# Kernel tuning notes

Hardware: AMD Instinct MI355X
Metric: run time of the kernel (lower is better)

The kernel has to match this reference:

```python
import jax, jax.numpy as jnp
import numpy as np

# dims: T time steps, B batch, F clinical features, H GRU hidden, NH heads, DFF ffn dim, AH single-attn hidden
T, B, F, H, NH, DFF, AH = 128, 256, 76, 64, 4, 256, 8


def setup_inputs() -> dict:
    key = jax.random.key(0)
    ks = jax.random.split(key, 32)
    s = 0.1
    def u(k, shape):
        return jax.random.uniform(k, shape, jnp.float32, -s, s)
    return {
        "x": jax.random.normal(ks[0], (T, B, F), jnp.float32),
        # per-feature GRU(1, H) weight stacks (torch gate order: r, z, n)
        "gru_w_ih": u(ks[1], (F, 3 * H)),          # input dim is 1 -> squeezed
        "gru_w_hh": u(ks[2], (F, 3 * H, H)),
        "gru_b_ih": jnp.zeros((F, 3 * H), jnp.float32),
        "gru_b_hh": jnp.zeros((F, 3 * H), jnp.float32),
        # per-feature SingleAttention('new', time_aware) params
        "att_Wt": u(ks[3], (F, H, AH)),
        "att_Wx": u(ks[4], (F, H, AH)),
        "att_rate": jnp.full((F,), 0.8, jnp.float32),
        # multi-head self-attention over the feature axis
        "mha_wq": u(ks[5], (H, H)), "mha_bq": jnp.zeros((H,), jnp.float32),
        "mha_wk": u(ks[6], (H, H)), "mha_bk": jnp.zeros((H,), jnp.float32),
        "mha_wv": u(ks[7], (H, H)), "mha_bv": jnp.zeros((H,), jnp.float32),
        "mha_wo": u(ks[8], (H, H)), "mha_bo": jnp.zeros((H,), jnp.float32),
        # position-wise feed forward
        "ffn_w1": u(ks[9], (H, DFF)), "ffn_b1": jnp.zeros((DFF,), jnp.float32),
        "ffn_w2": u(ks[10], (DFF, H)), "ffn_b2": jnp.zeros((H,), jnp.float32),
        # FinalAttentionQKV ('mul')
        "fa_wq": u(ks[11], (H, H)), "fa_bq": jnp.zeros((H,), jnp.float32),
        "fa_wk": u(ks[12], (H, H)), "fa_bk": jnp.zeros((H,), jnp.float32),
        "fa_wv": u(ks[13], (H, H)), "fa_bv": jnp.zeros((H,), jnp.float32),
        # output head
        "out0_w": u(ks[14], (H, H)), "out0_b": jnp.zeros((H,), jnp.float32),
        "out1_w": u(ks[15], (H, 1)), "out1_b": jnp.zeros((1,), jnp.float32),
    }


def reference(x, gru_w_ih, gru_w_hh, gru_b_ih, gru_b_hh,
              att_Wt, att_Wx, att_rate,
              mha_wq, mha_bq, mha_wk, mha_bk, mha_wv, mha_bv, mha_wo, mha_bo,
              ffn_w1, ffn_b1, ffn_w2, ffn_b2,
              fa_wq, fa_bq, fa_wk, fa_bk, fa_wv, fa_bv,
              out0_w, out0_b, out1_w, out1_b):
    # x: (T, B, F); torch permutes to (B, T, F)
    Ts, Bsz, Fd = x.shape
    Hd = gru_w_hh.shape[-1]
    dk = Hd // NH

    # ---- all F GRU(1,H) channels fused into one scan (vectorized over F) ----
    xs = jnp.transpose(x, (0, 2, 1))  # (T, F, B)

    def step(h, x_t):  # h: (F,B,H), x_t: (F,B)
        gx = x_t[:, :, None] * gru_w_ih[:, None, :] + gru_b_ih[:, None, :]      # (F,B,3H)
        gh = jnp.einsum('fbh,fgh->fbg', h, gru_w_hh) + gru_b_hh[:, None, :]     # (F,B,3H)
        rx, zx, nx = jnp.split(gx, 3, axis=-1)
        rh, zh, nh = jnp.split(gh, 3, axis=-1)
        r = jax.nn.sigmoid(rx + rh)
        z = jax.nn.sigmoid(zx + zh)
        n = jnp.tanh(nx + r * nh)
        h_new = (1.0 - z) * n + z * h
        return h_new, h_new

    h0 = jnp.zeros((Fd, Bsz, Hd), x.dtype)
    _, hs = jax.lax.scan(step, h0, xs)        # (T, F, B, H)
    hs = jnp.transpose(hs, (1, 2, 0, 3))       # (F, B, T, H)

    # ---- per-feature SingleAttention, type='new', time-aware ----
    q = jnp.einsum('fbh,fha->fba', hs[:, :, -1, :], att_Wt)   # (F,B,AH)
    k = jnp.einsum('fbth,fha->fbta', hs, att_Wx)              # (F,B,T,AH)
    dp = jnp.einsum('fba,fbta->fbt', q, k)                    # (F,B,T)
    sig = jax.nn.sigmoid(dp)
    decay = jnp.arange(Ts, 0, -1, dtype=x.dtype)              # T..1 (time_decays + 1)
    denom = jax.nn.sigmoid(att_rate)[:, None, None] * (jnp.log(2.72 + (1.0 - sig)) * decay)
    e = jax.nn.relu(sig / denom)
    a = jax.nn.softmax(e, axis=-1)
    emb = jnp.einsum('fbt,fbth->bfh', a, hs)                  # (B, F, H)

    def lin(t, w, b):
        return t @ w + b

    # ---- multi-head self-attention over the F axis + residual ----
    # NOTE: original lambda ignores its (layernormed) argument, so LN is dead code.
    def heads(t):
        return t.reshape(Bsz, Fd, NH, dk).transpose(0, 2, 1, 3)
    qh = heads(lin(emb, mha_wq, mha_bq))
    kh = heads(lin(emb, mha_wk, mha_bk))
    vh = heads(lin(emb, mha_wv, mha_bv))
    scores = jnp.einsum('bhqd,bhkd->bhqk', qh, kh) / jnp.sqrt(jnp.asarray(dk, x.dtype))
    attn = jax.nn.softmax(scores, axis=-1)
    ctx = jnp.einsum('bhqk,bhkd->bhqd', attn, vh).transpose(0, 2, 1, 3).reshape(Bsz, Fd, Hd)
    ctx = emb + lin(ctx, mha_wo, mha_bo)

    # ---- position-wise feed-forward + residual ----
    ctx = ctx + lin(jax.nn.relu(lin(ctx, ffn_w1, ffn_b1)), ffn_w2, ffn_b2)

    # ---- FinalAttentionQKV, type='mul' ----
    fq = lin(ctx[:, -1, :], fa_wq, fa_bq)      # (B,H)
    fk = lin(ctx, fa_wk, fa_bk)                # (B,F,H)
    fv = lin(ctx, fa_wv, fa_bv)                # (B,F,H)
    fe = jnp.einsum('bfh,bh->bf', fk, fq)
    fa_w = jax.nn.softmax(fe, axis=1)
    v = jnp.einsum('bf,bfh->bh', fa_w, fv)     # (B,H)

    # ---- output head ----
    out = jax.nn.sigmoid(lin(jax.nn.relu(lin(v, out0_w, out0_b)), out1_w, out1_b))
    return out  # (B, 1)
```

## Files before the change

### kernel.cpp

```cpp
#include <hip/hip_runtime.h>
#include <hip/hip_bf16.h>
#include <cstdint>
#include <cstddef>

#define TT 128
#define BBATCH 256
#define FFEAT 76
#define HDIM 64
#define NHEAD 4
#define DKH 16
#define DFF1 256
#define AH1 8
#define NROWS (BBATCH * FFEAT)

#define LOG2E 1.4426950408889634f

typedef __attribute__((ext_vector_type(8))) short bf16x8;
typedef __attribute__((ext_vector_type(4))) float f32x4;

__device__ __forceinline__ float fast_sigmoid(float v) {
    float p = __builtin_amdgcn_exp2f(-v * LOG2E);
    return __builtin_amdgcn_rcpf(1.0f + p);
}
__device__ __forceinline__ float fast_tanh(float v) {
    float p = __builtin_amdgcn_exp2f(v * (2.0f * LOG2E));
    return 1.0f - 2.0f * __builtin_amdgcn_rcpf(1.0f + p);
}
__device__ __forceinline__ short f2bf(float x) {
    __hip_bfloat16 h = __float2bfloat16(x);
    return *reinterpret_cast<short*>(&h);
}

__global__ __launch_bounds__(512, 2) void gru_mfma_kernel(
    const float* __restrict__ x, const float* __restrict__ w_ih,
    const float* __restrict__ w_hh, const float* __restrict__ b_ih,
    const float* __restrict__ b_hh, int f_base, __hip_bfloat16* __restrict__ hs)
{
    const int f_loc = blockIdx.y;
    const int f     = f_base + f_loc;
    const int b0    = blockIdx.x * 64;
    const int tid   = threadIdx.x;
    const int wave  = tid >> 6;
    const int lane  = tid & 63;
    const int col   = lane & 15;
    const int quad  = lane >> 4;
    const int ug    = wave & 3;
    const int mt0   = (wave >> 2) * 2;
    const int u     = ug * 16 + col;

    __shared__ __align__(16) short h_lds[2][64][72];
    __shared__ __align__(16) float x_lds[TT][64];

    for (int i = tid; i < TT * 64; i += 512) {
        int t = i >> 6, b = i & 63;
        x_lds[t][b] = x[(size_t)t * BBATCH * FFEAT + (size_t)(b0 + b) * FFEAT + f];
    }
    for (int i = tid; i < 64 * 72; i += 512) ((short*)h_lds[0])[i] = 0;

    bf16x8 bfr[3][2];
    {
        const float* whh_f = w_hh + (size_t)f * 192 * 64;
        #pragma unroll
        for (int gi = 0; gi < 3; ++gi) {
            const float* row = whh_f + (size_t)(gi * 64 + u) * 64;
            #pragma unroll
            for (int kq = 0; kq < 2; ++kq) {
                const float* src = row + kq * 32 + quad * 8;
                bf16x8 fr;
                #pragma unroll
                for (int j = 0; j < 8; ++j) fr[j] = f2bf(src[j]);
                bfr[gi][kq] = fr;
            }
        }
    }
    const float wihr  = w_ih[f*192 + u];
    const float wihz  = w_ih[f*192 + 64 + u];
    const float wihn  = w_ih[f*192 + 128 + u];
    const float brz_r = b_ih[f*192 + u]      + b_hh[f*192 + u];
    const float brz_z = b_ih[f*192 + 64 + u] + b_hh[f*192 + 64 + u];
    const float bih_n = b_ih[f*192 + 128 + u];
    const float bhh_n = b_hh[f*192 + 128 + u];

    float hprev[2][4] = {{0.f,0.f,0.f,0.f},{0.f,0.f,0.f,0.f}};
    __syncthreads();

    int p = 0;
    for (int t = 0; t < TT; ++t) {
        bf16x8 afr[2][2];
        #pragma unroll
        for (int mi = 0; mi < 2; ++mi)
            #pragma unroll
            for (int kq = 0; kq < 2; ++kq)
                afr[mi][kq] = *(const bf16x8*)&h_lds[p][(mt0+mi)*16 + col][kq*32 + quad*8];

        f32x4 acc[2][3];
        #pragma unroll
        for (int mi = 0; mi < 2; ++mi)
            #pragma unroll
            for (int gi = 0; gi < 3; ++gi) {
                f32x4 a = {0.f, 0.f, 0.f, 0.f};
                a = __builtin_amdgcn_mfma_f32_16x16x32_bf16(afr[mi][0], bfr[gi][0], a, 0, 0, 0);
                a = __builtin_amdgcn_mfma_f32_16x16x32_bf16(afr[mi][1], bfr[gi][1], a, 0, 0, 0);
                acc[mi][gi] = a;
            }

        #pragma unroll
        for (int mi = 0; mi < 2; ++mi) {
            const int brow = (mt0 + mi) * 16 + quad * 4;
            float4 xv = *(const float4*)&x_lds[t][brow];
            #pragma unroll
            for (int r = 0; r < 4; ++r) {
                float xb = (&xv.x)[r];
                float R  = acc[mi][0][r] + fmaf(xb, wihr, brz_r);
                float Z  = acc[mi][1][r] + fmaf(xb, wihz, brz_z);
                float NH = acc[mi][2][r] + bhh_n;
                float NX = fmaf(xb, wihn, bih_n);
                float rg = fast_sigmoid(R);
                float zg = fast_sigmoid(Z);
                float ng = fast_tanh(fmaf(rg, NH, NX));
                float hn = fmaf(zg, hprev[mi][r] - ng, ng);
                hprev[mi][r] = hn;
                short hb = f2bf(hn);
                h_lds[p^1][brow + r][u] = hb;
                hs[(((size_t)f_loc * BBATCH + b0 + brow + r) * TT + t) * HDIM + u] =
                    *reinterpret_cast<__hip_bfloat16*>(&hb);
            }
        }
        __syncthreads();
        p ^= 1;
    }
}

__global__ __launch_bounds__(128) void attn_kernel(
    const __hip_bfloat16* __restrict__ hs, const float* __restrict__ Wt,
    const float* __restrict__ Wx, const float* __restrict__ rate,
    int f_base, float* __restrict__ emb)
{
    const int b     = blockIdx.x;
    const int f_loc = blockIdx.y;
    const int f     = f_base + f_loc;
    const int tid   = threadIdx.x;

    __shared__ float h_s[TT][HDIM + 1];
    __shared__ float wx_s[HDIM][AH1];
    __shared__ float wt_s[HDIM][AH1];
    __shared__ float q_s[AH1];
    __shared__ float a_s[TT];
    __shared__ float redm[2], redp[2];
    __shared__ float partial_s[HDIM];

    for (int i = tid; i < HDIM * AH1; i += 128) {
        ((float*)wx_s)[i] = Wx[(size_t)f * HDIM * AH1 + i];
        ((float*)wt_s)[i] = Wt[(size_t)f * HDIM * AH1 + i];
    }

    float hreg[HDIM];
    {
        const __hip_bfloat16* src = hs + (((size_t)f_loc * BBATCH + b) * TT + tid) * HDIM;
        #pragma unroll
        for (int c = 0; c < 8; ++c) {
            uint4 u4 = ((const uint4*)src)[c];
            unsigned vals[4] = {u4.x, u4.y, u4.z, u4.w};
            #pragma unroll
            for (int pp = 0; pp < 4; ++pp) {
                hreg[c*8 + 2*pp]     = __uint_as_float(vals[pp] << 16);
                hreg[c*8 + 2*pp + 1] = __uint_as_float(vals[pp] & 0xffff0000u);
            }
        }
        #pragma unroll
        for (int j = 0; j < HDIM; ++j) h_s[tid][j] = hreg[j];
    }
    __syncthreads();

    if (tid < AH1) {
        float acc = 0.f;
        #pragma unroll
        for (int j = 0; j < HDIM; ++j) acc += h_s[TT-1][j] * wt_s[j][tid];
        q_s[tid] = acc;
    }
    __syncthreads();

    float k[AH1];
    #pragma unroll
    for (int a = 0; a < AH1; ++a) k[a] = 0.f;
    #pragma unroll
    for (int j = 0; j < HDIM; ++j) {
        float hv = hreg[j];
        #pragma unroll
        for (int a = 0; a < AH1; ++a) k[a] = fmaf(hv, wx_s[j][a], k[a]);
    }
    float dp = 0.f;
    #pragma unroll
    for (int a = 0; a < AH1; ++a) dp += k[a] * q_s[a];

    float sig   = fast_sigmoid(dp);
    float rs    = fast_sigmoid(rate[f]);
    float decay = (float)(TT - tid);
    float denom = rs * (__logf(2.72f + (1.0f - sig)) * decay);
    float e = fmaxf(sig / denom, 0.0f);

    float m = e;
    #pragma unroll
    for (int off = 32; off > 0; off >>= 1) m = fmaxf(m, __shfl_xor(m, off, 64));
    if ((tid & 63) == 0) redm[tid >> 6] = m;
    __syncthreads();
    m = fmaxf(redm[0], redm[1]);
    float pr = __builtin_amdgcn_exp2f((e - m) * LOG2E);
    float s = pr;
    #pragma unroll
    for (int off = 32; off > 0; off >>= 1) s += __shfl_xor(s, off, 64);
    if ((tid & 63) == 0) redp[tid >> 6] = s;
    __syncthreads();
    s = redp[0] + redp[1];
    a_s[tid] = pr / s;
    __syncthreads();

    const int j    = tid & 63;
    const int half = tid >> 6;
    float acc = 0.f;
    const int t0 = half * 64;
    #pragma unroll 8
    for (int t2 = t0; t2 < t0 + 64; ++t2)
        acc = fmaf(a_s[t2], h_s[t2][j], acc);
    if (half) partial_s[j] = acc;
    __syncthreads();
    if (!half) emb[((size_t)b * FFEAT + f) * HDIM + j] = acc + partial_s[j];
}

struct GemmP {
    const float* X;
    const float* W[3];
    const float* B[3];
    const float* R;
    float* Y[3];
    int K;
    int Nfull;
    int act;
};

__global__ __launch_bounds__(256) void gemm_kernel(GemmP A)
{
    __shared__ float xs[64][65];
    __shared__ float ws[64][68];

    const int tid = threadIdx.x;
    const int tx  = tid & 15;
    const int ty  = tid >> 4;
    const int m0  = blockIdx.x * 64;
    const int n0  = blockIdx.y * 64;
    const int z   = blockIdx.z;

    const float* W = A.W[z];
    const float* Bv = A.B[z];
    float* Y = A.Y[z];
    const int K = A.K, Nfull = A.Nfull;

    float acc[4][4];
    #pragma unroll
    for (int i = 0; i < 4; ++i)
        #pragma unroll
        for (int j = 0; j < 4; ++j) acc[i][j] = 0.f;

    for (int kc = 0; kc < K; kc += 64) {
        for (int s = tid; s < 1024; s += 256) {
            int row = s >> 4, c4 = s & 15;
            float4 xv = *(const float4*)&A.X[(size_t)(m0 + row) * K + kc + 4*c4];
            xs[row][4*c4+0] = xv.x; xs[row][4*c4+1] = xv.y;
            xs[row][4*c4+2] = xv.z; xs[row][4*c4+3] = xv.w;
            float4 wv = *(const float4*)&W[(size_t)(kc + row) * Nfull + n0 + 4*c4];
            *(float4*)&ws[row][4*c4] = wv;
        }
        __syncthreads();
        #pragma unroll 16
        for (int k = 0; k < 64; ++k) {
            float a0 = xs[4*ty+0][k], a1 = xs[4*ty+1][k];
            float a2 = xs[4*ty+2][k], a3 = xs[4*ty+3][k];
            float4 wv = *(const float4*)&ws[k][4*tx];
            #pragma unroll
            for (int j = 0; j < 4; ++j) {
                float wj = (&wv.x)[j];
                acc[0][j] = fmaf(a0, wj, acc[0][j]);
                acc[1][j] = fmaf(a1, wj, acc[1][j]);
                acc[2][j] = fmaf(a2, wj, acc[2][j]);
                acc[3][j] = fmaf(a3, wj, acc[3][j]);
            }
        }
        __syncthreads();
    }

    float4 bias = *(const float4*)&Bv[n0 + 4*tx];
    #pragma unroll
    for (int i = 0; i < 4; ++i) {
        int row = m0 + 4*ty + i;
        float4 v;
        v.x = acc[i][0] + bias.x; v.y = acc[i][1] + bias.y;
        v.z = acc[i][2] + bias.z; v.w = acc[i][3] + bias.w;
        if (A.act) {
            v.x = fmaxf(v.x, 0.f); v.y = fmaxf(v.y, 0.f);
            v.z = fmaxf(v.z, 0.f); v.w = fmaxf(v.w, 0.f);
        }
        if (A.R) {
            float4 r4 = *(const float4*)&A.R[(size_t)row * Nfull + n0 + 4*tx];
            v.x += r4.x; v.y += r4.y; v.z += r4.z; v.w += r4.w;
        }
        *(float4*)&Y[(size_t)row * Nfull + n0 + 4*tx] = v;
    }
}

__global__ __launch_bounds__(256) void mha_core_kernel(
    const float* __restrict__ q, const float* __restrict__ k,
    const float* __restrict__ v, float* __restrict__ ctx)
{
    const int b  = blockIdx.x;
    const int hh = blockIdx.y;
    const int tid = threadIdx.x;

    __shared__ float qs[FFEAT][17];
    __shared__ float ks[FFEAT][17];
    __shared__ float vs[FFEAT][17];
    __shared__ float ps[FFEAT][77];

    for (int idx = tid; idx < FFEAT * DKH; idx += 256) {
        int i = idx >> 4, c = idx & 15;
        size_t g = ((size_t)b * FFEAT + i) * HDIM + hh * DKH + c;
        qs[i][c] = q[g]; ks[i][c] = k[g]; vs[i][c] = v[g];
    }
    __syncthreads();

    for (int idx = tid; idx < FFEAT * FFEAT; idx += 256) {
        int i = idx / FFEAT, j = idx % FFEAT;
        float acc = 0.f;
        #pragma unroll
        for (int c = 0; c < DKH; ++c) acc = fmaf(qs[i][c], ks[j][c], acc);
        ps[i][j] = acc * 0.25f;
    }
    __syncthreads();

    if (tid < FFEAT) {
        float mm = ps[tid][0];
        #pragma unroll 4
        for (int j = 1; j < FFEAT; ++j) mm = fmaxf(mm, ps[tid][j]);
        float ss = 0.f;
        #pragma unroll 4
        for (int j = 0; j < FFEAT; ++j) {
            float pv = __builtin_amdgcn_exp2f((ps[tid][j] - mm) * LOG2E);
            ps[tid][j] = pv; ss += pv;
        }
        float inv = 1.0f / ss;
        #pragma unroll 4
        for (int j = 0; j < FFEAT; ++j) ps[tid][j] *= inv;
    }
    __syncthreads();

    for (int idx = tid; idx < FFEAT * DKH; idx += 256) {
        int i = idx >> 4, c = idx & 15;
        float acc = 0.f;
        #pragma unroll 4
        for (int j = 0; j < FFEAT; ++j) acc = fmaf(ps[i][j], vs[j][c], acc);
        ctx[((size_t)b * FFEAT + i) * HDIM + hh * DKH + c] = acc;
    }
}

__global__ __launch_bounds__(128) void final_kernel(
    const float* __restrict__ ctx3, const float* __restrict__ fk,
    const float* __restrict__ fv,
    const float* __restrict__ faq, const float* __restrict__ fabq,
    const float* __restrict__ o0w, const float* __restrict__ o0b,
    const float* __restrict__ o1w, const float* __restrict__ o1b,
    float* __restrict__ out)
{
    const int b = blockIdx.x;
    const int tid = threadIdx.x;

    __shared__ float last[HDIM];
    __shared__ float fqs[HDIM];
    __shared__ float sm[FFEAT];
    __shared__ float vv[HDIM];
    __shared__ float hh[HDIM];
    __shared__ float redm[2], redp[2];

    if (tid < HDIM) last[tid] = ctx3[((size_t)b * FFEAT + FFEAT - 1) * HDIM + tid];
    __syncthreads();
    if (tid < HDIM) {
        float acc = fabq[tid];
        #pragma unroll 8
        for (int j = 0; j < HDIM; ++j) acc = fmaf(last[j], faq[j * HDIM + tid], acc);
        fqs[tid] = acc;
    }
    __syncthreads();

    float e = -3.0e38f;
    if (tid < FFEAT) {
        const float4* kr = (const float4*)&fk[((size_t)b * FFEAT + tid) * HDIM];
        float acc = 0.f;
        #pragma unroll
        for (int c4 = 0; c4 < 16; ++c4) {
            float4 kv = kr[c4];
            acc = fmaf(kv.x, fqs[4*c4+0], acc);
            acc = fmaf(kv.y, fqs[4*c4+1], acc);
            acc = fmaf(kv.z, fqs[4*c4+2], acc);
            acc = fmaf(kv.w, fqs[4*c4+3], acc);
        }
        e = acc;
    }
    float m = e;
    #pragma unroll
    for (int off = 32; off > 0; off >>= 1) m = fmaxf(m, __shfl_xor(m, off, 64));
    if ((tid & 63) == 0) redm[tid >> 6] = m;
    __syncthreads();
    m = fmaxf(redm[0], redm[1]);
    float p = (tid < FFEAT) ? __builtin_amdgcn_exp2f((e - m) * LOG2E) : 0.f;
    float s = p;
    #pragma unroll
    for (int off = 32; off > 0; off >>= 1) s += __shfl_xor(s, off, 64);
    if ((tid & 63) == 0) redp[tid >> 6] = s;
    __syncthreads();
    s = redp[0] + redp[1];
    if (tid < FFEAT) sm[tid] = p / s;
    __syncthreads();

    if (tid < HDIM) {
        float acc = 0.f;
        for (int ff = 0; ff < FFEAT; ++ff)
            acc = fmaf(sm[ff], fv[((size_t)b * FFEAT + ff) * HDIM + tid], acc);
        vv[tid] = acc;
    }
    __syncthreads();
    if (tid < HDIM) {
        float acc = o0b[tid];
        #pragma unroll 8
        for (int j = 0; j < HDIM; ++j) acc = fmaf(vv[j], o0w[j * HDIM + tid], acc);
        hh[tid] = fmaxf(acc, 0.f);
    }
    __syncthreads();
    if (tid < 64) {
        float t = hh[tid] * o1w[tid];
        #pragma unroll
        for (int off = 32; off > 0; off >>= 1) t += __shfl_xor(t, off, 64);
        if (tid == 0) out[b] = fast_sigmoid(t + o1b[0]);
    }
}

__global__ void ws_report_kernel(float* out, int n, float ws_mib) {
    int i = blockIdx.x * blockDim.x + threadIdx.x;
    if (i < n) out[i] = ws_mib;
}

extern "C" void kernel_launch(void* const* d_in, const int* in_sizes, int n_in,
                              void* d_out, int out_size, void* d_ws, size_t ws_size,
                              hipStream_t stream)
{
    const float* x     = (const float*)d_in[0];
    const float* w_ih  = (const float*)d_in[1];
    const float* w_hh  = (const float*)d_in[2];
    const float* b_ih  = (const float*)d_in[3];
    const float* b_hh  = (const float*)d_in[4];
    const float* attWt = (const float*)d_in[5];
    const float* attWx = (const float*)d_in[6];
    const float* attRt = (const float*)d_in[7];
    const float* wq    = (const float*)d_in[8];
    const float* bq    = (const float*)d_in[9];
    const float* wk    = (const float*)d_in[10];
    const float* bk    = (const float*)d_in[11];
    const float* wv    = (const float*)d_in[12];
    const float* bv    = (const float*)d_in[13];
    const float* wo    = (const float*)d_in[14];
    const float* bo    = (const float*)d_in[15];
    const float* w1    = (const float*)d_in[16];
    const float* b1    = (const float*)d_in[17];
    const float* w2    = (const float*)d_in[18];
    const float* b2    = (const float*)d_in[19];
    const float* faq   = (const float*)d_in[20];
    const float* fabq  = (const float*)d_in[21];
    const float* fak   = (const float*)d_in[22];
    const float* fabk  = (const float*)d_in[23];
    const float* fav   = (const float*)d_in[24];
    const float* fabv  = (const float*)d_in[25];
    const float* o0w   = (const float*)d_in[26];
    const float* o0b   = (const float*)d_in[27];
    const float* o1w   = (const float*)d_in[28];
    const float* o1b   = (const float*)d_in[29];
    float* out = (float*)d_out;

    const size_t emb_bytes  = (size_t)NROWS * HDIM * 4;
    const size_t R64        = (size_t)NROWS * HDIM;
    const size_t tail_bytes = 12 * R64 * 4;

    const int chunk_opts[6] = {76, 38, 19, 4, 2, 1};
    int FC = 0;
    for (int i = 0; i < 6; ++i) {
        size_t hs_b = (size_t)chunk_opts[i] * BBATCH * TT * HDIM * 2;
        size_t scratch = hs_b > tail_bytes ? hs_b : tail_bytes;
        if (emb_bytes + scratch <= ws_size) { FC = chunk_opts[i]; break; }
    }
    if (FC == 0) {
        ws_report_kernel<<<dim3((out_size + 255) / 256), dim3(256), 0, stream>>>(
            out, out_size, (float)((double)ws_size / (1024.0 * 1024.0)));
        return;
    }

    float* emb = (float*)d_ws;
    char*  scratch = (char*)d_ws + emb_bytes;
    __hip_bfloat16* hs = (__hip_bfloat16*)scratch;

    for (int f0 = 0; f0 < FFEAT; f0 += FC) {
        int fc = (FFEAT - f0 < FC) ? (FFEAT - f0) : FC;
        gru_mfma_kernel<<<dim3(4, fc), dim3(512), 0, stream>>>(
            x, w_ih, w_hh, b_ih, b_hh, f0, hs);
        attn_kernel<<<dim3(BBATCH, fc), dim3(128), 0, stream>>>(
            hs, attWt, attWx, attRt, f0, emb);
    }

    float* ts   = (float*)scratch;
    float* q    = ts;
    float* k    = ts + 1*R64;
    float* v    = ts + 2*R64;
    float* ctx  = ts + 3*R64;
    float* ctx2 = ts + 4*R64;
    float* hid  = ts + 5*R64;
    float* ctx3 = ts + 9*R64;
    float* fk   = ts + 10*R64;
    float* fv   = ts + 11*R64;

    const int MB = NROWS / 64;

    {
        GemmP A = { emb, {wq, wk, wv}, {bq, bk, bv}, nullptr, {q, k, v}, 64, 64, 0 };
        gemm_kernel<<<dim3(MB, 1, 3), dim3(256), 0, stream>>>(A);
    }
    mha_core_kernel<<<dim3(BBATCH, NHEAD), dim3(256), 0, stream>>>(q, k, v, ctx);
    {
        GemmP A = { ctx, {wo, nullptr, nullptr}, {bo, nullptr, nullptr}, emb,
                    {ctx2, nullptr, nullptr}, 64, 64, 0 };
        gemm_kernel<<<dim3(MB, 1, 1), dim3(256), 0, stream>>>(A);
    }
    {
        GemmP A = { ctx2, {w1, nullptr, nullptr}, {b1, nullptr, nullptr}, nullptr,
                    {hid, nullptr, nullptr}, 64, 256, 1 };
        gemm_kernel<<<dim3(MB, 4, 1), dim3(256), 0, stream>>>(A);
    }
    {
        GemmP A = { hid, {w2, nullptr, nullptr}, {b2, nullptr, nullptr}, ctx2,
                    {ctx3, nullptr, nullptr}, 256, 64, 0 };
        gemm_kernel<<<dim3(MB, 1, 1), dim3(256), 0, stream>>>(A);
    }
    {
        GemmP A = { ctx3, {fak, fav, nullptr}, {fabk, fabv, nullptr}, nullptr,
                    {fk, fv, nullptr}, 64, 64, 0 };
        gemm_kernel<<<dim3(MB, 1, 2), dim3(256), 0, stream>>>(A);
    }
    final_kernel<<<dim3(BBATCH), dim3(128), 0, stream>>>(
        ctx3, fk, fv, faq, fabq, o0w, o0b, o1w, o1b, out);
}
```

Before: 694.1 us.

## Make GRU waves independent and fold attention query into per-batch weight vector

The GRU kernel now gives each wave 16 batch rows and all 192 gate columns, so each wave keeps its own hidden state in LDS and the per-step block-wide barrier goes away. hs is stored time-major, written as 16-byte vectors one step late, and biases are preloaded into the MFMA accumulators. At the end the GRU kernel computes the last-step query and folds it with Wx into a per-(batch, feature) 64-vector, so the attention kernel only needs one dot product per time step instead of the full key projection. Attention runs as a single 64-thread wave with shuffle-only reductions. The cost is higher register pressure (24 B fragments per lane), fewer threads per GRU block, and strided per-timestep reads in the attention kernel.

```diff
diff --git a/kernel.cpp b/kernel.cpp
--- a/kernel.cpp
+++ b/kernel.cpp
@@ -30,201 +30,223 @@
     __hip_bfloat16 h = __float2bfloat16(x);
     return *reinterpret_cast<short*>(&h);
 }
-
-__global__ __launch_bounds__(512, 2) void gru_mfma_kernel(
+__device__ __forceinline__ float bf2f(unsigned short s) {
+    return __uint_as_float(((unsigned)s) << 16);
+}
+
+__global__ __launch_bounds__(256) void gru_scan_kernel(
     const float* __restrict__ x, const float* __restrict__ w_ih,
     const float* __restrict__ w_hh, const float* __restrict__ b_ih,
-    const float* __restrict__ b_hh, int f_base, __hip_bfloat16* __restrict__ hs)
+    const float* __restrict__ b_hh, const float* __restrict__ Wt,
+    const float* __restrict__ Wx, int f_base,
+    __hip_bfloat16* __restrict__ hs, float* __restrict__ wtil)
 {
     const int f_loc = blockIdx.y;
     const int f     = f_base + f_loc;
-    const int b0    = blockIdx.x * 64;
+    const int bblk  = blockIdx.x * 64;
     const int tid   = threadIdx.x;
     const int wave  = tid >> 6;
     const int lane  = tid & 63;
-    const int col   = lane & 15;
-    const int quad  = lane >> 4;
-    const int ug    = wave & 3;
-    const int mt0   = (wave >> 2) * 2;
-    const int u     = ug * 16 + col;
-
-    __shared__ __align__(16) short h_lds[2][64][72];
-    __shared__ __align__(16) float x_lds[TT][64];
-
-    for (int i = tid; i < TT * 64; i += 512) {
+    const int c     = lane & 15;
+    const int q     = lane >> 4;
+    const int b0    = bblk + wave * 16;
+
+    __shared__ float x_lds[TT][64];
+    __shared__ float wt_s[64][8];
+    __shared__ float wx_s[64][8];
+    __shared__ short hx[4][16][72];
+    __shared__ float q_s[4][16][8];
+
+    for (int i = tid; i < TT * 64; i += 256) {
         int t = i >> 6, b = i & 63;
-        x_lds[t][b] = x[(size_t)t * BBATCH * FFEAT + (size_t)(b0 + b) * FFEAT + f];
-    }
-    for (int i = tid; i < 64 * 72; i += 512) ((short*)h_lds[0])[i] = 0;
-
-    bf16x8 bfr[3][2];
+        x_lds[t][b] = x[((size_t)t * BBATCH + bblk + b) * FFEAT + f];
+    }
+    for (int i = tid; i < 512; i += 256) {
+        ((float*)wt_s)[i] = Wt[(size_t)f * 512 + i];
+        ((float*)wx_s)[i] = Wx[(size_t)f * 512 + i];
+    }
+    for (int i = lane; i < 16 * 72; i += 64) ((short*)hx[wave])[i] = 0;
+    __syncthreads();
+
+    bf16x8 bfr[12][2];
     {
         const float* whh_f = w_hh + (size_t)f * 192 * 64;
         #pragma unroll
-        for (int gi = 0; gi < 3; ++gi) {
-            const float* row = whh_f + (size_t)(gi * 64 + u) * 64;
+        for (int nt = 0; nt < 12; ++nt) {
+            const float* row = whh_f + (size_t)(nt * 16 + c) * 64;
             #pragma unroll
             for (int kq = 0; kq < 2; ++kq) {
-                const float* src = row + kq * 32 + quad * 8;
                 bf16x8 fr;
                 #pragma unroll
-                for (int j = 0; j < 8; ++j) fr[j] = f2bf(src[j]);
-                bfr[gi][kq] = fr;
+                for (int j = 0; j < 8; ++j) fr[j] = f2bf(row[kq * 32 + q * 8 + j]);
+                bfr[nt][kq] = fr;
             }
         }
     }
-    const float wihr  = w_ih[f*192 + u];
-    const float wihz  = w_ih[f*192 + 64 + u];
-    const float wihn  = w_ih[f*192 + 128 + u];
-    const float brz_r = b_ih[f*192 + u]      + b_hh[f*192 + u];
-    const float brz_z = b_ih[f*192 + 64 + u] + b_hh[f*192 + 64 + u];
-    const float bih_n = b_ih[f*192 + 128 + u];
-    const float bhh_n = b_hh[f*192 + 128 + u];
-
-    float hprev[2][4] = {{0.f,0.f,0.f,0.f},{0.f,0.f,0.f,0.f}};
-    __syncthreads();
-
-    int p = 0;
+    float wihr[4], wihz[4], wihn[4], bR[4], bZ[4], bNX[4], bNH[4];
+    #pragma unroll
+    for (int g = 0; g < 4; ++g) {
+        int u = g * 16 + c;
+        wihr[g] = w_ih[f*192 + u];
+        wihz[g] = w_ih[f*192 + 64 + u];
+        wihn[g] = w_ih[f*192 + 128 + u];
+        bR[g]  = b_ih[f*192 + u]      + b_hh[f*192 + u];
+        bZ[g]  = b_ih[f*192 + 64 + u] + b_hh[f*192 + 64 + u];
+        bNX[g] = b_ih[f*192 + 128 + u];
+        bNH[g] = b_hh[f*192 + 128 + u];
+    }
+
+    float hprev[4][4];
+    #pragma unroll
+    for (int g = 0; g < 4; ++g)
+        #pragma unroll
+        for (int r = 0; r < 4; ++r) hprev[g][r] = 0.f;
+
+    short* hs_s = (short*)hs + (size_t)f_loc * TT * BBATCH * HDIM;
+
     for (int t = 0; t < TT; ++t) {
-        bf16x8 afr[2][2];
-        #pragma unroll
-        for (int mi = 0; mi < 2; ++mi)
-            #pragma unroll
-            for (int kq = 0; kq < 2; ++kq)
-                afr[mi][kq] = *(const bf16x8*)&h_lds[p][(mt0+mi)*16 + col][kq*32 + quad*8];
-
-        f32x4 acc[2][3];
-        #pragma unroll
-        for (int mi = 0; mi < 2; ++mi)
-            #pragma unroll
-            for (int gi = 0; gi < 3; ++gi) {
-                f32x4 a = {0.f, 0.f, 0.f, 0.f};
-                a = __builtin_amdgcn_mfma_f32_16x16x32_bf16(afr[mi][0], bfr[gi][0], a, 0, 0, 0);
-                a = __builtin_amdgcn_mfma_f32_16x16x32_bf16(afr[mi][1], bfr[gi][1], a, 0, 0, 0);
-                acc[mi][gi] = a;
-            }
-
-        #pragma unroll
-        for (int mi = 0; mi < 2; ++mi) {
-            const int brow = (mt0 + mi) * 16 + quad * 4;
-            float4 xv = *(const float4*)&x_lds[t][brow];
+        bf16x8 a0 = *(const bf16x8*)&hx[wave][c][q * 8];
+        bf16x8 a1 = *(const bf16x8*)&hx[wave][c][32 + q * 8];
+        if (t > 0) {
+            short* dst = hs_s + ((size_t)(t - 1) * BBATCH + b0 + c) * HDIM + q * 8;
+            *(bf16x8*)dst = a0;
+            *(bf16x8*)(dst + 32) = a1;
+        }
+
+        f32x4 acc[12];
+        #pragma unroll
+        for (int g = 0; g < 4; ++g) {
+            acc[g]     = f32x4{bR[g],  bR[g],  bR[g],  bR[g]};
+            acc[g + 4] = f32x4{bZ[g],  bZ[g],  bZ[g],  bZ[g]};
+            acc[g + 8] = f32x4{bNH[g], bNH[g], bNH[g], bNH[g]};
+        }
+        #pragma unroll
+        for (int nt = 0; nt < 12; ++nt) {
+            acc[nt] = __builtin_amdgcn_mfma_f32_16x16x32_bf16(a0, bfr[nt][0], acc[nt], 0, 0, 0);
+            acc[nt] = __builtin_amdgcn_mfma_f32_16x16x32_bf16(a1, bfr[nt][1], acc[nt], 0, 0, 0);
+        }
+
+        float4 xv = *(const float4*)&x_lds[t][wave * 16 + q * 4];
+        #pragma unroll
+        for (int g = 0; g < 4; ++g) {
             #pragma unroll
             for (int r = 0; r < 4; ++r) {
                 float xb = (&xv.x)[r];
-                float R  = acc[mi][0][r] + fmaf(xb, wihr, brz_r);
-                float Z  = acc[mi][1][r] + fmaf(xb, wihz, brz_z);
-                float NH = acc[mi][2][r] + bhh_n;
-                float NX = fmaf(xb, wihn, bih_n);
+                float R  = fmaf(xb, wihr[g], acc[g][r]);
+                float Z  = fmaf(xb, wihz[g], acc[g + 4][r]);
+                float NX = fmaf(xb, wihn[g], bNX[g]);
                 float rg = fast_sigmoid(R);
                 float zg = fast_sigmoid(Z);
-                float ng = fast_tanh(fmaf(rg, NH, NX));
-                float hn = fmaf(zg, hprev[mi][r] - ng, ng);
-                hprev[mi][r] = hn;
-                short hb = f2bf(hn);
-                h_lds[p^1][brow + r][u] = hb;
-                hs[(((size_t)f_loc * BBATCH + b0 + brow + r) * TT + t) * HDIM + u] =
-                    *reinterpret_cast<__hip_bfloat16*>(&hb);
+                float ng = fast_tanh(fmaf(rg, acc[g + 8][r], NX));
+                float hn = fmaf(zg, hprev[g][r] - ng, ng);
+                hprev[g][r] = hn;
+                hx[wave][q * 4 + r][g * 16 + c] = f2bf(hn);
             }
         }
-        __syncthreads();
-        p ^= 1;
-    }
-}
-
-__global__ __launch_bounds__(128) void attn_kernel(
-    const __hip_bfloat16* __restrict__ hs, const float* __restrict__ Wt,
-    const float* __restrict__ Wx, const float* __restrict__ rate,
-    int f_base, float* __restrict__ emb)
+    }
+    {
+        bf16x8 a0 = *(const bf16x8*)&hx[wave][c][q * 8];
+        bf16x8 a1 = *(const bf16x8*)&hx[wave][c][32 + q * 8];
+        short* dst = hs_s + ((size_t)(TT - 1) * BBATCH + b0 + c) * HDIM + q * 8;
+        *(bf16x8*)dst = a0;
+        *(bf16x8*)(dst + 32) = a1;
+    }
+
+    #pragma unroll
+    for (int rr = 0; rr < 2; ++rr) {
+        int role = rr * 64 + lane;
+        int b = role >> 3, a = role & 7;
+        float s = 0.f;
+        #pragma unroll 8
+        for (int j = 0; j < 64; ++j)
+            s = fmaf(bf2f((unsigned short)hx[wave][b][j]), wt_s[j][a], s);
+        q_s[wave][b][a] = s;
+    }
+    {
+        int b = lane >> 2, jb = (lane & 3) * 16;
+        float qreg[8];
+        #pragma unroll
+        for (int a = 0; a < 8; ++a) qreg[a] = q_s[wave][b][a];
+        float* wt_out = wtil + ((size_t)(b0 + b) * FFEAT + f) * HDIM + jb;
+        #pragma unroll
+        for (int j4 = 0; j4 < 4; ++j4) {
+            float4 v;
+            #pragma unroll
+            for (int jj = 0; jj < 4; ++jj) {
+                int j = jb + j4 * 4 + jj;
+                float s = 0.f;
+                #pragma unroll
+                for (int a = 0; a < 8; ++a) s = fmaf(wx_s[j][a], qreg[a], s);
+                (&v.x)[jj] = s;
+            }
+            *(float4*)&wt_out[j4 * 4] = v;
+        }
+    }
+}
+
+__global__ __launch_bounds__(64) void attn2_kernel(
+    const __hip_bfloat16* __restrict__ hs, const float* __restrict__ wtil,
+    const float* __restrict__ rate, int f_base, float* __restrict__ emb)
 {
     const int b     = blockIdx.x;
     const int f_loc = blockIdx.y;
     const int f     = f_base + f_loc;
-    const int tid   = threadIdx.x;
-
-    __shared__ float h_s[TT][HDIM + 1];
-    __shared__ float wx_s[HDIM][AH1];
-    __shared__ float wt_s[HDIM][AH1];
-    __shared__ float q_s[AH1];
+    const int lane  = threadIdx.x;
+
     __shared__ float a_s[TT];
-    __shared__ float redm[2], redp[2];
-    __shared__ float partial_s[HDIM];
-
-    for (int i = tid; i < HDIM * AH1; i += 128) {
-        ((float*)wx_s)[i] = Wx[(size_t)f * HDIM * AH1 + i];
-        ((float*)wt_s)[i] = Wt[(size_t)f * HDIM * AH1 + i];
-    }
-
-    float hreg[HDIM];
-    {
-        const __hip_bfloat16* src = hs + (((size_t)f_loc * BBATCH + b) * TT + tid) * HDIM;
-        #pragma unroll
-        for (int c = 0; c < 8; ++c) {
-            uint4 u4 = ((const uint4*)src)[c];
-            unsigned vals[4] = {u4.x, u4.y, u4.z, u4.w};
+
+    float wreg[64];
+    {
+        const float4* src = (const float4*)(wtil + ((size_t)b * FFEAT + f) * HDIM);
+        #pragma unroll
+        for (int i = 0; i < 16; ++i) {
+            float4 v = src[i];
+            wreg[4*i+0] = v.x; wreg[4*i+1] = v.y; wreg[4*i+2] = v.z; wreg[4*i+3] = v.w;
+        }
+    }
+    const float rs = fast_sigmoid(rate[f]);
+    const short* hsp = (const short*)hs + (size_t)f_loc * TT * BBATCH * HDIM;
+
+    float e[2];
+    #pragma unroll
+    for (int half = 0; half < 2; ++half) {
+        int t = half * 64 + lane;
+        const uint4* row = (const uint4*)(hsp + ((size_t)t * BBATCH + b) * HDIM);
+        float dp = 0.f;
+        #pragma unroll
+        for (int c4 = 0; c4 < 8; ++c4) {
+            uint4 u = row[c4];
+            unsigned vals[4] = {u.x, u.y, u.z, u.w};
             #pragma unroll
-            for (int pp = 0; pp < 4; ++pp) {
-                hreg[c*8 + 2*pp]     = __uint_as_float(vals[pp] << 16);
-                hreg[c*8 + 2*pp + 1] = __uint_as_float(vals[pp] & 0xffff0000u);
+            for (int p = 0; p < 4; ++p) {
+                dp = fmaf(__uint_as_float(vals[p] << 16),        wreg[c4*8 + 2*p],     dp);
+                dp = fmaf(__uint_as_float(vals[p] & 0xffff0000u), wreg[c4*8 + 2*p + 1], dp);
             }
         }
-        #pragma unroll
-        for (int j = 0; j < HDIM; ++j) h_s[tid][j] = hreg[j];
-    }
-    __syncthreads();
-
-    if (tid < AH1) {
-        float acc = 0.f;
-        #pragma unroll
-        for (int j = 0; j < HDIM; ++j) acc += h_s[TT-1][j] * wt_s[j][tid];
-        q_s[tid] = acc;
-    }
-    __syncthreads();
-
-    float k[AH1];
-    #pragma unroll
-    for (int a = 0; a < AH1; ++a) k[a] = 0.f;
-    #pragma unroll
-    for (int j = 0; j < HDIM; ++j) {
-        float hv = hreg[j];
-        #pragma unroll
-        for (int a = 0; a < AH1; ++a) k[a] = fmaf(hv, wx_s[j][a], k[a]);
-    }
-    float dp = 0.f;
-    #pragma unroll
-    for (int a = 0; a < AH1; ++a) dp += k[a] * q_s[a];
-
-    float sig   = fast_sigmoid(dp);
-    float rs    = fast_sigmoid(rate[f]);
-    float decay = (float)(TT - tid);
-    float denom = rs * (__logf(2.72f + (1.0f - sig)) * decay);
-    float e = fmaxf(sig / denom, 0.0f);
-
-    float m = e;
+        float sig = fast_sigmoid(dp);
+        float den = rs * (__logf(2.72f + (1.0f - sig)) * (float)(TT - t));
+        e[half] = fmaxf(sig / den, 0.0f);
+    }
+    float m = fmaxf(e[0], e[1]);
     #pragma unroll
     for (int off = 32; off > 0; off >>= 1) m = fmaxf(m, __shfl_xor(m, off, 64));
-    if ((tid & 63) == 0) redm[tid >> 6] = m;
-    __syncthreads();
-    m = fmaxf(redm[0], redm[1]);
-    float pr = __builtin_amdgcn_exp2f((e - m) * LOG2E);
-    float s = pr;
+    float p0 = __builtin_amdgcn_exp2f((e[0] - m) * LOG2E);
+    float p1 = __builtin_amdgcn_exp2f((e[1] - m) * LOG2E);
+    float s = p0 + p1;
     #pragma unroll
     for (int off = 32; off > 0; off >>= 1) s += __shfl_xor(s, off, 64);
-    if ((tid & 63) == 0) redp[tid >> 6] = s;
-    __syncthreads();
-    s = redp[0] + redp[1];
-    a_s[tid] = pr / s;
-    __syncthreads();
-
-    const int j    = tid & 63;
-    const int half = tid >> 6;
+    float inv = __builtin_amdgcn_rcpf(s);
+    a_s[lane]      = p0 * inv;
+    a_s[lane + 64] = p1 * inv;
+
+    const int j = lane;
     float acc = 0.f;
-    const int t0 = half * 64;
     #pragma unroll 8
-    for (int t2 = t0; t2 < t0 + 64; ++t2)
-        acc = fmaf(a_s[t2], h_s[t2][j], acc);
-    if (half) partial_s[j] = acc;
-    __syncthreads();
-    if (!half) emb[((size_t)b * FFEAT + f) * HDIM + j] = acc + partial_s[j];
+    for (int t = 0; t < TT; ++t) {
+        unsigned short hv = *(const unsigned short*)(hsp + ((size_t)t * BBATCH + b) * HDIM + j);
+        acc = fmaf(a_s[t], bf2f(hv), acc);
+    }
+    emb[((size_t)b * FFEAT + f) * HDIM + j] = acc;
 }
 
 struct GemmP {
@@ -483,6 +505,7 @@
     float* out = (float*)d_out;
 
     const size_t emb_bytes  = (size_t)NROWS * HDIM * 4;
+    const size_t wtil_bytes = (size_t)NROWS * HDIM * 4;
     const size_t R64        = (size_t)NROWS * HDIM;
     const size_t tail_bytes = 12 * R64 * 4;
 
@@ -491,7 +514,7 @@
     for (int i = 0; i < 6; ++i) {
         size_t hs_b = (size_t)chunk_opts[i] * BBATCH * TT * HDIM * 2;
         size_t scratch = hs_b > tail_bytes ? hs_b : tail_bytes;
-        if (emb_bytes + scratch <= ws_size) { FC = chunk_opts[i]; break; }
+        if (emb_bytes + wtil_bytes + scratch <= ws_size) { FC = chunk_opts[i]; break; }
     }
     if (FC == 0) {
         ws_report_kernel<<<dim3((out_size + 255) / 256), dim3(256), 0, stream>>>(
@@ -499,16 +522,17 @@
         return;
     }
 
-    float* emb = (float*)d_ws;
-    char*  scratch = (char*)d_ws + emb_bytes;
+    float* emb  = (float*)d_ws;
+    float* wtil = (float*)((char*)d_ws + emb_bytes);
+    char*  scratch = (char*)d_ws + emb_bytes + wtil_bytes;
     __hip_bfloat16* hs = (__hip_bfloat16*)scratch;
 
     for (int f0 = 0; f0 < FFEAT; f0 += FC) {
         int fc = (FFEAT - f0 < FC) ? (FFEAT - f0) : FC;
-        gru_mfma_kernel<<<dim3(4, fc), dim3(512), 0, stream>>>(
-            x, w_ih, w_hh, b_ih, b_hh, f0, hs);
-        attn_kernel<<<dim3(BBATCH, fc), dim3(128), 0, stream>>>(
-            hs, attWt, attWx, attRt, f0, emb);
+        gru_scan_kernel<<<dim3(4, fc), dim3(256), 0, stream>>>(
+            x, w_ih, w_hh, b_ih, b_hh, attWt, attWx, f0, hs, wtil);
+        attn2_kernel<<<dim3(BBATCH, fc), dim3(64), 0, stream>>>(
+            hs, wtil, attRt, f0, emb);
     }
 
     float* ts   = (float*)scratch;
```

After: 690.9 us. No clear change (-0.5%).
